# Kernel tuning notes

Measured on AMD Instinct MI355X. Metric: run time of the kernel, lower is better.

## Reference

```python
import jax, jax.numpy as jnp
import numpy as np

B, S, D, R, H = 4, 2048, 1024, 256, 8
NI, NP, NO, K = 8, 32, 8, 3
DH = R // H


def _householder_chain(x, vs):
    # x: [B,S,R], vs: [B,S,K,R]; apply K Householder reflections sequentially
    def step(carry, v):
        vn = v * jax.lax.rsqrt(jnp.sum(v * v, axis=-1, keepdims=True) + 1e-8)
        vTx = jnp.sum(carry * vn, axis=-1, keepdims=True)
        return carry - 2.0 * vn * vTx, None
    out, _ = jax.lax.scan(step, x, jnp.moveaxis(vs, 2, 0))
    return out


def _circuit_down(x, in_neurons, proc_neurons, input_weights, proc_idx):
    # soft mixture of input-neuron projections: d_model -> rank
    all_proj = jnp.einsum('bsd,ndr->bsnr', x, in_neurons)
    xr = jnp.einsum('bsnr,bsn->bsr', all_proj, input_weights)
    return _householder_chain(xr, proc_neurons[proc_idx])


def setup_inputs():
    key = jax.random.key(0)
    ks = jax.random.split(key, 14)
    n = lambda k, shape, sc: jax.random.normal(k, shape, jnp.float32) * sc
    inv_d, inv_r = 1.0 / np.sqrt(D), 1.0 / np.sqrt(R)
    return {
        'x': n(ks[0], (B, S, D), 1.0),
        'q_in': n(ks[1], (NI, D, R), inv_d),
        'q_proc': n(ks[2], (NP, R), inv_r),
        'k_in': n(ks[3], (NI, D, R), inv_d),
        'k_proc': n(ks[4], (NP, R), inv_r),
        'v_in': n(ks[5], (NI, D, R), inv_d),
        'v_proc': n(ks[6], (NP, R), inv_r),
        'o_proc': n(ks[7], (NP, R), inv_r),
        'o_out': n(ks[8], (NO, R, D), inv_r),
        'rd_in': n(ks[9], (NI, D), inv_d),
        'rd_proc': n(ks[10], (NP, D), inv_d),
        'ru_out': n(ks[11], (NO, R), inv_r),
        'ru_proc': n(ks[12], (NP, R), inv_r),
    }


def reference(x, q_in, q_proc, k_in, k_proc, v_in, v_proc, o_proc, o_out,
              rd_in, rd_proc, ru_out, ru_proc):
    # --- router (down): soft input weights + top-k process indices ---
    input_weights = jax.nn.softmax(x @ rd_in.T, axis=-1)          # [B,S,NI]
    _, pidx = jax.lax.top_k(x @ rd_proc.T, K)                     # [B,S,K]

    q = _circuit_down(x, q_in, q_proc, input_weights, pidx)      # [B,S,R]
    k = _circuit_down(x, k_in, k_proc, input_weights, pidx)
    v = _circuit_down(x, v_in, v_proc, input_weights, pidx)

    qh = q.reshape(B, S, H, DH)
    kh = k.reshape(B, S, H, DH)
    vh = v.reshape(B, S, H, DH)
    scores = jnp.einsum('bqhd,bkhd->bhqk', qh, kh) / np.sqrt(DH)
    attn = jax.nn.softmax(scores, axis=-1)
    o = jnp.einsum('bhqk,bkhd->bqhd', attn, vh).reshape(B, S, R)  # [B,S,R]

    # --- router (up): soft output weights + top-k process indices ---
    output_weights = jax.nn.softmax(o @ ru_out.T, axis=-1)        # [B,S,NO]
    _, pidx_u = jax.lax.top_k(o @ ru_proc.T, K)                   # [B,S,K]

    oh = _householder_chain(o, o_proc[pidx_u])                    # [B,S,R]
    out = jnp.einsum('bsr,bsn,nrd->bsd', oh, output_weights, o_out)
    return out
```

## Files before the change

kernel.cpp:

```cpp
#include <hip/hip_runtime.h>
#include <math.h>

#define NI 8
#define NP 32
#define TOPK 3

typedef _Float16 f16;
typedef f16 f16x8 __attribute__((ext_vector_type(8)));
typedef f16 f16x4 __attribute__((ext_vector_type(4)));
typedef float f32x4 __attribute__((ext_vector_type(4)));

__device__ __forceinline__ float wave_sum(float v) {
  #pragma unroll
  for (int off = 32; off; off >>= 1) v += __shfl_xor(v, off);
  return v;
}

__device__ __forceinline__ void gload16(const void* g, void* l) {
  __builtin_amdgcn_global_load_lds(
      (const __attribute__((address_space(1))) unsigned int*)g,
      (__attribute__((address_space(3))) unsigned int*)l, 16, 0, 0);
}

__device__ __forceinline__ void split4(float4 v, f16x4& h, f16x4& l) {
  h[0] = (f16)v.x; l[0] = (f16)(v.x - (float)h[0]);
  h[1] = (f16)v.y; l[1] = (f16)(v.y - (float)h[1]);
  h[2] = (f16)v.z; l[2] = (f16)(v.z - (float)h[2]);
  h[3] = (f16)v.w; l[3] = (f16)(v.w - (float)h[3]);
}

template<int CHUNKS>
__global__ __launch_bounds__(256) void router_v2(
    const float* __restrict__ X,
    const float* __restrict__ Wsm,
    const float* __restrict__ Wtk,
    float* __restrict__ iw, int* __restrict__ pidx,
    f16* __restrict__ Xh, f16* __restrict__ Xl)
{
  const int Kin = CHUNKS * 256;
  const int tid = threadIdx.x, wave = tid >> 6, lane = tid & 63;
  __shared__ float sc[4][4][40];
  const size_t t0 = (size_t)blockIdx.x * 16 + wave * 4;

  float4 xv[4][CHUNKS];
  #pragma unroll
  for (int tt = 0; tt < 4; ++tt) {
    const float4* Xp = reinterpret_cast<const float4*>(X + (t0 + tt) * Kin);
    #pragma unroll
    for (int c = 0; c < CHUNKS; ++c) xv[tt][c] = Xp[c * 64 + lane];
  }
  if (Xh) {
    #pragma unroll
    for (int tt = 0; tt < 4; ++tt)
      #pragma unroll
      for (int c = 0; c < CHUNKS; ++c) {
        f16x4 h, l;
        split4(xv[tt][c], h, l);
        size_t off = (t0 + tt) * Kin + (c * 64 + lane) * 4;
        *reinterpret_cast<f16x4*>(Xh + off) = h;
        *reinterpret_cast<f16x4*>(Xl + off) = l;
      }
  }

  for (int w = 0; w < 40; ++w) {
    const float* Wr = (w < NI) ? (Wsm + (size_t)w * Kin) : (Wtk + (size_t)(w - NI) * Kin);
    const float4* Wp = reinterpret_cast<const float4*>(Wr);
    float p[4] = {};
    #pragma unroll
    for (int c = 0; c < CHUNKS; ++c) {
      float4 wv = Wp[c * 64 + lane];
      #pragma unroll
      for (int tt = 0; tt < 4; ++tt) {
        p[tt] = fmaf(xv[tt][c].x, wv.x, p[tt]);
        p[tt] = fmaf(xv[tt][c].y, wv.y, p[tt]);
        p[tt] = fmaf(xv[tt][c].z, wv.z, p[tt]);
        p[tt] = fmaf(xv[tt][c].w, wv.w, p[tt]);
      }
    }
    #pragma unroll
    for (int tt = 0; tt < 4; ++tt) {
      p[tt] = wave_sum(p[tt]);
      if (lane == 0) sc[wave][tt][w] = p[tt];
    }
  }

  for (int tt = 0; tt < 4; ++tt) {
    float s = (lane < NI) ? sc[wave][tt][lane] : -3.0e38f;
    float m = s;
    #pragma unroll
    for (int off = 4; off; off >>= 1) m = fmaxf(m, __shfl_xor(m, off));
    float e = expf(s - m);
    float sum = e;
    #pragma unroll
    for (int off = 4; off; off >>= 1) sum += __shfl_xor(sum, off);
    if (lane < NI) iw[(t0 + tt) * NI + lane] = e / sum;

    float v = (lane < NP) ? sc[wave][tt][NI + lane] : -3.0e38f;
    int idx = lane;
    #pragma unroll
    for (int j = 0; j < TOPK; ++j) {
      float bv = v; int bi = idx;
      #pragma unroll
      for (int off = 32; off; off >>= 1) {
        float ov = __shfl_xor(bv, off); int oi = __shfl_xor(bi, off);
        if (ov > bv || (ov == bv && oi < bi)) { bv = ov; bi = oi; }
      }
      if (lane == 0) pidx[(t0 + tt) * TOPK + j] = bi;
      if (idx == bi) v = -3.0e38f;
    }
  }
}

__global__ __launch_bounds__(256) void pack_bt(
    const float* __restrict__ S, f16* __restrict__ Dh, f16* __restrict__ Dl,
    int C, int K)
{
  __shared__ float T[64][65];
  const int tid = threadIdx.x;
  const int kb = blockIdx.x * 64, cb = blockIdx.y * 64;
  const int tr = tid >> 4, tc = (tid & 15) * 4;
  #pragma unroll
  for (int i = 0; i < 4; ++i) {
    float4 v = *reinterpret_cast<const float4*>(&S[(size_t)(kb + tr + i * 16) * C + cb + tc]);
    T[tr + i * 16][tc + 0] = v.x; T[tr + i * 16][tc + 1] = v.y;
    T[tr + i * 16][tc + 2] = v.z; T[tr + i * 16][tc + 3] = v.w;
  }
  __syncthreads();
  #pragma unroll
  for (int i = 0; i < 4; ++i) {
    int c = tr + i * 16;
    f16x4 vh, vl;
    #pragma unroll
    for (int q = 0; q < 4; ++q) {
      float a = T[tc + q][c];
      f16 h = (f16)a;
      vh[q] = h;
      vl[q] = (f16)(a - (float)h);
    }
    *reinterpret_cast<f16x4*>(&Dh[(size_t)(cb + c) * K + kb + tc]) = vh;
    *reinterpret_cast<f16x4*>(&Dl[(size_t)(cb + c) * K + kb + tc]) = vl;
  }
}

#define TBM 128
#define TBN 128
#define TBK 32

__global__ __launch_bounds__(256, 3) void gemm_split2(
    const f16* __restrict__ Xh, const f16* __restrict__ Xl, int Kin,
    const float* __restrict__ W,
    const f16* __restrict__ Bth, const f16* __restrict__ Btl,
    float* __restrict__ C, int ldC, int Ktot, int n_pass)
{
  __shared__ f16x8 AhL[512];
  __shared__ f16x8 AlL[512];
  __shared__ f16x8 BhL[512];
  __shared__ f16x8 BlL[512];
  __shared__ float Ws[TBM][NI];

  const int tid = threadIdx.x;
  const int wave = tid >> 6, lane = tid & 63;
  const int wm = wave >> 1, wn = wave & 1;
  const int fr = lane & 15, ks = lane >> 4;
  const int row0 = blockIdx.x * TBM, c0 = blockIdx.y * TBN;
  const int n_base = blockIdx.z * n_pass;
  const int koff = n_base * Kin;

  for (int i = tid; i < TBM * NI; i += 256)
    Ws[i >> 3][i & 7] = W[(size_t)(row0 + (i >> 3)) * NI + (i & 7)];

  const int s1 = 256 + tid;
  const int ar0 = tid >> 2, kg0 = ((tid & 3) - (ar0 >> 1)) & 3;
  const int ar1 = s1 >> 2,  kg1 = ((s1 & 3) - (ar1 >> 1)) & 3;

  const f16* xh0 = Xh + (size_t)(row0 + ar0) * Kin + kg0 * 8;
  const f16* xh1 = Xh + (size_t)(row0 + ar1) * Kin + kg1 * 8;
  const f16* xl0 = Xl + (size_t)(row0 + ar0) * Kin + kg0 * 8;
  const f16* xl1 = Xl + (size_t)(row0 + ar1) * Kin + kg1 * 8;
  const f16* bh0 = Bth + (size_t)(c0 + ar0) * Ktot + koff + kg0 * 8;
  const f16* bh1 = Bth + (size_t)(c0 + ar1) * Ktot + koff + kg1 * 8;
  const f16* bl0 = Btl + (size_t)(c0 + ar0) * Ktot + koff + kg0 * 8;
  const f16* bl1 = Btl + (size_t)(c0 + ar1) * Ktot + koff + kg1 * 8;

  f16x8* AhW = &AhL[wave * 64];
  f16x8* AlW = &AlL[wave * 64];
  f16x8* BhW = &BhL[wave * 64];
  f16x8* BlW = &BlL[wave * 64];

  f32x4 acc[4][4] = {};
  f32x4 cac[4][4] = {};

  int n = n_base, dk0 = 0;
  const int Kloc = n_pass * Kin;
  for (int kt = 0; kt < Kloc; kt += TBK) {
    __syncthreads();
    gload16(xh0 + dk0, AhW);
    gload16(xh1 + dk0, AhW + 256);
    gload16(xl0 + dk0, AlW);
    gload16(xl1 + dk0, AlW + 256);
    gload16(bh0 + kt, BhW);
    gload16(bh1 + kt, BhW + 256);
    gload16(bl0 + kt, BlW);
    gload16(bl1 + kt, BlW + 256);
    __syncthreads();

    f16x8 ah[4], al[4], bh[4], bl[4];
    #pragma unroll
    for (int mf = 0; mf < 4; ++mf) {
      int ar = wm * 64 + mf * 16 + fr;
      int sl = ar * 4 + (((ar >> 1) + ks) & 3);
      ah[mf] = AhL[sl]; al[mf] = AlL[sl];
    }
    #pragma unroll
    for (int nf = 0; nf < 4; ++nf) {
      int bc = wn * 64 + nf * 16 + fr;
      int sl = bc * 4 + (((bc >> 1) + ks) & 3);
      bh[nf] = BhL[sl]; bl[nf] = BlL[sl];
    }
    #pragma unroll
    for (int mf = 0; mf < 4; ++mf)
      #pragma unroll
      for (int nf = 0; nf < 4; ++nf) {
        acc[mf][nf] = __builtin_amdgcn_mfma_f32_16x16x32_f16(ah[mf], bh[nf], acc[mf][nf], 0, 0, 0);
        acc[mf][nf] = __builtin_amdgcn_mfma_f32_16x16x32_f16(ah[mf], bl[nf], acc[mf][nf], 0, 0, 0);
        acc[mf][nf] = __builtin_amdgcn_mfma_f32_16x16x32_f16(al[mf], bh[nf], acc[mf][nf], 0, 0, 0);
      }

    dk0 += TBK;
    if (dk0 == Kin) {
      dk0 = 0;
      #pragma unroll
      for (int mf = 0; mf < 4; ++mf) {
        float w0 = Ws[wm * 64 + mf * 16 + ks * 4 + 0][n];
        float w1 = Ws[wm * 64 + mf * 16 + ks * 4 + 1][n];
        float w2 = Ws[wm * 64 + mf * 16 + ks * 4 + 2][n];
        float w3 = Ws[wm * 64 + mf * 16 + ks * 4 + 3][n];
        #pragma unroll
        for (int nf = 0; nf < 4; ++nf) {
          cac[mf][nf][0] = fmaf(w0, acc[mf][nf][0], cac[mf][nf][0]);
          cac[mf][nf][1] = fmaf(w1, acc[mf][nf][1], cac[mf][nf][1]);
          cac[mf][nf][2] = fmaf(w2, acc[mf][nf][2], cac[mf][nf][2]);
          cac[mf][nf][3] = fmaf(w3, acc[mf][nf][3], cac[mf][nf][3]);
          acc[mf][nf] = (f32x4){0.f, 0.f, 0.f, 0.f};
        }
      }
      ++n;
    }
  }

  #pragma unroll
  for (int mf = 0; mf < 4; ++mf)
    #pragma unroll
    for (int nf = 0; nf < 4; ++nf) {
      int col = c0 + wn * 64 + nf * 16 + fr;
      #pragma unroll
      for (int j = 0; j < 4; ++j) {
        int row = row0 + wm * 64 + mf * 16 + ks * 4 + j;
        atomicAdd(&C[(size_t)row * ldC + col], cac[mf][nf][j]);
      }
    }
}

#define GBM 128
#define GBN 128
#define GBK 16
#define GBMp 132

__global__ __launch_bounds__(256) void gemm_mix(
    const float* __restrict__ X, int Kin,
    const float* __restrict__ W,
    const float* __restrict__ Bm0, const float* __restrict__ Bm1, const float* __restrict__ Bm2,
    int ldB, float* __restrict__ C, int ldC, int Nz)
{
  __shared__ float As[GBK][GBMp];
  __shared__ float Bs[GBK][GBMp];
  __shared__ float Ws[GBM][NI];
  const int tid = threadIdx.x;
  const int row0 = blockIdx.x * GBM;
  const int z = blockIdx.z;
  const float* Bm = (z == 0) ? Bm0 : (z == 1) ? Bm1 : Bm2;
  const int c0 = blockIdx.y * GBN;
  for (int i = tid; i < GBM * NI; i += 256)
    Ws[i >> 3][i & 7] = W[(size_t)(row0 + (i >> 3)) * NI + (i & 7)];
  __syncthreads();

  float acc[8][8] = {};
  const int tr = tid >> 4, tc = tid & 15;
  const int srow = tid >> 2;
  const int sseg = (tid & 3) * 4;
  const int bk = tid >> 4;
  const int bc = (tid & 15) * 4;

  const int Ktot = Kin * NI;
  int n = 0, dk0 = 0;
  for (int kt = 0; kt < Ktot; kt += GBK) {
    __syncthreads();
    #pragma unroll
    for (int p = 0; p < 2; ++p) {
      int r = p * 64 + srow;
      float4 xv = *reinterpret_cast<const float4*>(&X[(size_t)(row0 + r) * Kin + dk0 + sseg]);
      float wgt = Ws[r][n];
      As[sseg + 0][r] = xv.x * wgt;
      As[sseg + 1][r] = xv.y * wgt;
      As[sseg + 2][r] = xv.z * wgt;
      As[sseg + 3][r] = xv.w * wgt;
    }
    #pragma unroll
    for (int p = 0; p < 2; ++p) {
      int cc = p * 64 + bc;
      float4 bv = *reinterpret_cast<const float4*>(&Bm[(size_t)(kt + bk) * ldB + c0 + cc]);
      *reinterpret_cast<float4*>(&Bs[bk][cc]) = bv;
    }
    __syncthreads();
    #pragma unroll
    for (int k = 0; k < GBK; ++k) {
      float4 a0 = *reinterpret_cast<const float4*>(&As[k][tr * 8]);
      float4 a1 = *reinterpret_cast<const float4*>(&As[k][tr * 8 + 4]);
      float4 b0 = *reinterpret_cast<const float4*>(&Bs[k][tc * 8]);
      float4 b1 = *reinterpret_cast<const float4*>(&Bs[k][tc * 8 + 4]);
      float av[8] = {a0.x, a0.y, a0.z, a0.w, a1.x, a1.y, a1.z, a1.w};
      float bv[8] = {b0.x, b0.y, b0.z, b0.w, b1.x, b1.y, b1.z, b1.w};
      #pragma unroll
      for (int i = 0; i < 8; ++i)
        #pragma unroll
        for (int j = 0; j < 8; ++j)
          acc[i][j] = fmaf(av[i], bv[j], acc[i][j]);
    }
    dk0 += GBK;
    if (dk0 == Kin) { dk0 = 0; ++n; }
  }
  #pragma unroll
  for (int i = 0; i < 8; ++i) {
    int row = row0 + tr * 8 + i;
    float* Cp = C + (size_t)row * ldC + z * Nz + c0 + tc * 8;
    float4 o0 = {acc[i][0], acc[i][1], acc[i][2], acc[i][3]};
    float4 o1 = {acc[i][4], acc[i][5], acc[i][6], acc[i][7]};
    *reinterpret_cast<float4*>(Cp) = o0;
    *reinterpret_cast<float4*>(Cp + 4) = o1;
  }
}

__global__ __launch_bounds__(256) void hh_kernel(
    float* __restrict__ X, int ldX,
    const float* __restrict__ P0, const float* __restrict__ P1, const float* __restrict__ P2,
    const int* __restrict__ pidx,
    f16* __restrict__ D0h, f16* __restrict__ D0l,
    f16* __restrict__ D1h, f16* __restrict__ D1l,
    f16* __restrict__ D2h, f16* __restrict__ D2l)
{
  const int tid = threadIdx.x, wave = tid >> 6, lane = tid & 63;
  const int t = blockIdx.x * 4 + wave;
  const int circ = blockIdx.y;
  const float* P = (circ == 0) ? P0 : (circ == 1) ? P1 : P2;
  float* xp = X + (size_t)t * ldX + circ * 256;
  float4 x4 = *reinterpret_cast<float4*>(xp + lane * 4);
  #pragma unroll
  for (int j = 0; j < TOPK; ++j) {
    int id = pidx[t * TOPK + j];
    const float* vp = P + (size_t)id * 256;
    float4 v4 = *reinterpret_cast<const float4*>(vp + lane * 4);
    float ss = v4.x * v4.x + v4.y * v4.y + v4.z * v4.z + v4.w * v4.w;
    ss = wave_sum(ss);
    float inv = 1.0f / sqrtf(ss + 1e-8f);
    float4 vn = {v4.x * inv, v4.y * inv, v4.z * inv, v4.w * inv};
    float dt = vn.x * x4.x + vn.y * x4.y + vn.z * x4.z + vn.w * x4.w;
    dt = wave_sum(dt);
    float d2 = 2.0f * dt;
    x4.x = fmaf(-d2, vn.x, x4.x);
    x4.y = fmaf(-d2, vn.y, x4.y);
    x4.z = fmaf(-d2, vn.z, x4.z);
    x4.w = fmaf(-d2, vn.w, x4.w);
  }
  f16* Dh = (circ == 0) ? D0h : (circ == 1) ? D1h : D2h;
  f16* Dl = (circ == 0) ? D0l : (circ == 1) ? D1l : D2l;
  if (Dh) {
    f16x4 h, l;
    split4(x4, h, l);
    *reinterpret_cast<f16x4*>(Dh + (size_t)t * 256 + lane * 4) = h;
    *reinterpret_cast<f16x4*>(Dl + (size_t)t * 256 + lane * 4) = l;
  } else {
    *reinterpret_cast<float4*>(xp + lane * 4) = x4;
  }
}

__global__ __launch_bounds__(256, 2) void attn_mfma2(
    const float* __restrict__ qkv,
    const f16* __restrict__ Khg, const f16* __restrict__ Klg,
    const f16* __restrict__ Vhg, const f16* __restrict__ Vlg,
    float* __restrict__ O)
{
  __shared__ f16 Kh[64][40], Kl[64][40];
  __shared__ f16 Vh[32][72], Vl[32][72];
  __shared__ f16 Ph[4][32][72], Pl[4][32][72];

  const int tid = threadIdx.x, wave = tid >> 6, lane = tid & 63;
  const int c = lane & 15, g = lane >> 4;
  const int bh = blockIdx.y, b = bh >> 3, h = bh & 7;
  const int q0 = blockIdx.x * 128;
  const size_t tbase = (size_t)b * 2048;
  const float SCALE = 0.17677669529663687f;

  f16x8 qh[2], ql[2];
  #pragma unroll
  for (int qt = 0; qt < 2; ++qt) {
    const int row = q0 + wave * 32 + qt * 16 + c;
    const float* qp = qkv + (tbase + row) * 768 + h * 32 + g * 8;
    float4 a = *reinterpret_cast<const float4*>(qp);
    float4 b4 = *reinterpret_cast<const float4*>(qp + 4);
    float qv[8] = {a.x, a.y, a.z, a.w, b4.x, b4.y, b4.z, b4.w};
    #pragma unroll
    for (int j = 0; j < 8; ++j) {
      float xs = qv[j] * SCALE;
      f16 hh = (f16)xs;
      qh[qt][j] = hh;
      ql[qt][j] = (f16)(xs - (float)hh);
    }
  }

  f32x4 sacc[2][4];
  f32x4 oacc[2][2] = {};
  float mrow[2][4] = {{-INFINITY, -INFINITY, -INFINITY, -INFINITY},
                      {-INFINITY, -INFINITY, -INFINITY, -INFINITY}};
  float lrow[2][4] = {};

  for (int k0 = 0; k0 < 2048; k0 += 64) {
    __syncthreads();
    {
      const int kj = tid >> 2, dq = (tid & 3) * 8;
      const size_t krow = (tbase + k0 + kj) * 256 + h * 32 + dq;
      *reinterpret_cast<f16x8*>(&Kh[kj][dq]) = *reinterpret_cast<const f16x8*>(Khg + krow);
      *reinterpret_cast<f16x8*>(&Kl[kj][dq]) = *reinterpret_cast<const f16x8*>(Klg + krow);

      const int vk = tid & 63, vq = (tid >> 6) * 8;
      const size_t vrow = (tbase + k0 + vk) * 256 + h * 32 + vq;
      f16x8 vh8 = *reinterpret_cast<const f16x8*>(Vhg + vrow);
      f16x8 vl8 = *reinterpret_cast<const f16x8*>(Vlg + vrow);
      #pragma unroll
      for (int j = 0; j < 8; ++j) { Vh[vq + j][vk] = vh8[j]; Vl[vq + j][vk] = vl8[j]; }
    }
    __syncthreads();

    #pragma unroll
    for (int s = 0; s < 4; ++s) {
      f16x8 kbh = *reinterpret_cast<const f16x8*>(&Kh[s * 16 + c][g * 8]);
      f16x8 kbl = *reinterpret_cast<const f16x8*>(&Kl[s * 16 + c][g * 8]);
      #pragma unroll
      for (int qt = 0; qt < 2; ++qt) {
        f32x4 acc = {0.f, 0.f, 0.f, 0.f};
        acc = __builtin_amdgcn_mfma_f32_16x16x32_f16(qh[qt], kbh, acc, 0, 0, 0);
        acc = __builtin_amdgcn_mfma_f32_16x16x32_f16(qh[qt], kbl, acc, 0, 0, 0);
        acc = __builtin_amdgcn_mfma_f32_16x16x32_f16(ql[qt], kbh, acc, 0, 0, 0);
        sacc[qt][s] = acc;
      }
    }

    float alpha[2][4];
    #pragma unroll
    for (int qt = 0; qt < 2; ++qt)
      #pragma unroll
      for (int r = 0; r < 4; ++r) {
        float mt = fmaxf(fmaxf(sacc[qt][0][r], sacc[qt][1][r]),
                         fmaxf(sacc[qt][2][r], sacc[qt][3][r]));
        #pragma unroll
        for (int off = 1; off < 16; off <<= 1) mt = fmaxf(mt, __shfl_xor(mt, off));
        float mn = fmaxf(mrow[qt][r], mt);
        float al = __expf(mrow[qt][r] - mn);
        mrow[qt][r] = mn;
        alpha[qt][r] = al;
        float ps = 0.f;
        #pragma unroll
        for (int s = 0; s < 4; ++s) {
          float p = __expf(sacc[qt][s][r] - mn);
          sacc[qt][s][r] = p;
          ps += p;
        }
        #pragma unroll
        for (int off = 1; off < 16; off <<= 1) ps += __shfl_xor(ps, off);
        lrow[qt][r] = lrow[qt][r] * al + ps;
      }

    #pragma unroll
    for (int qt = 0; qt < 2; ++qt)
      #pragma unroll
      for (int s = 0; s < 4; ++s)
        #pragma unroll
        for (int r = 0; r < 4; ++r) {
          float p = sacc[qt][s][r];
          f16 hh = (f16)p;
          Ph[wave][qt * 16 + g * 4 + r][s * 16 + c] = hh;
          Pl[wave][qt * 16 + g * 4 + r][s * 16 + c] = (f16)(p - (float)hh);
        }

    #pragma unroll
    for (int qt = 0; qt < 2; ++qt)
      #pragma unroll
      for (int dh = 0; dh < 2; ++dh)
        #pragma unroll
        for (int r = 0; r < 4; ++r) oacc[qt][dh][r] *= alpha[qt][r];

    #pragma unroll
    for (int ch = 0; ch < 2; ++ch) {
      f16x8 pah[2], pal[2];
      #pragma unroll
      for (int qt = 0; qt < 2; ++qt) {
        pah[qt] = *reinterpret_cast<const f16x8*>(&Ph[wave][qt * 16 + c][ch * 32 + g * 8]);
        pal[qt] = *reinterpret_cast<const f16x8*>(&Pl[wave][qt * 16 + c][ch * 32 + g * 8]);
      }
      #pragma unroll
      for (int dh = 0; dh < 2; ++dh) {
        f16x8 vh = *reinterpret_cast<const f16x8*>(&Vh[dh * 16 + c][ch * 32 + g * 8]);
        f16x8 vl = *reinterpret_cast<const f16x8*>(&Vl[dh * 16 + c][ch * 32 + g * 8]);
        #pragma unroll
        for (int qt = 0; qt < 2; ++qt) {
          oacc[qt][dh] = __builtin_amdgcn_mfma_f32_16x16x32_f16(pah[qt], vh, oacc[qt][dh], 0, 0, 0);
          oacc[qt][dh] = __builtin_amdgcn_mfma_f32_16x16x32_f16(pah[qt], vl, oacc[qt][dh], 0, 0, 0);
          oacc[qt][dh] = __builtin_amdgcn_mfma_f32_16x16x32_f16(pal[qt], vh, oacc[qt][dh], 0, 0, 0);
        }
      }
    }
  }

  #pragma unroll
  for (int qt = 0; qt < 2; ++qt)
    #pragma unroll
    for (int r = 0; r < 4; ++r) {
      float inv = 1.0f / lrow[qt][r];
      int row = q0 + wave * 32 + qt * 16 + g * 4 + r;
      #pragma unroll
      for (int dh = 0; dh < 2; ++dh)
        O[(tbase + row) * 256 + h * 32 + dh * 16 + c] = oacc[qt][dh][r] * inv;
    }
}

__global__ __launch_bounds__(256) void attn_kernel(
    const float* __restrict__ qkv, float* __restrict__ O)
{
  const int tid = threadIdx.x;
  const int wave = tid >> 6, lane = tid & 63;
  const int bh = blockIdx.y, b = bh >> 3, h = bh & 7;
  const int q0 = blockIdx.x * 8;
  const size_t tbase = (size_t)b * 2048;
  const float SCALE = 0.17677669529663687f;

  __shared__ float Ks[64][36];
  __shared__ float Vt[32][68];
  __shared__ float Ps[4][2][64];

  const int wq = __builtin_amdgcn_readfirstlane(wave);
  const float* qr0 = qkv + (tbase + q0 + wq * 2) * 768 + h * 32;
  float qa[32], qb[32];
  #pragma unroll
  for (int i = 0; i < 32; ++i) { qa[i] = qr0[i]; qb[i] = qr0[768 + i]; }

  const int r = lane >> 5, d = lane & 31;
  float m0 = -INFINITY, m1 = -INFINITY, l0 = 0.f, l1 = 0.f, oacc = 0.f;

  for (int k0 = 0; k0 < 2048; k0 += 64) {
    __syncthreads();
    {
      int j = tid >> 2;
      int c = (tid & 3) * 8;
      const float* kp = qkv + (tbase + k0 + j) * 768 + 256 + h * 32 + c;
      float4 ka = *reinterpret_cast<const float4*>(kp);
      float4 kb = *reinterpret_cast<const float4*>(kp + 4);
      *reinterpret_cast<float4*>(&Ks[j][c]) = ka;
      *reinterpret_cast<float4*>(&Ks[j][c + 4]) = kb;
      const float* vp = qkv + (tbase + k0 + j) * 768 + 512 + h * 32 + c;
      float4 va = *reinterpret_cast<const float4*>(vp);
      float4 vb = *reinterpret_cast<const float4*>(vp + 4);
      Vt[c + 0][j] = va.x; Vt[c + 1][j] = va.y; Vt[c + 2][j] = va.z; Vt[c + 3][j] = va.w;
      Vt[c + 4][j] = vb.x; Vt[c + 5][j] = vb.y; Vt[c + 6][j] = vb.z; Vt[c + 7][j] = vb.w;
    }
    __syncthreads();
    float s0 = 0.f, s1 = 0.f;
    #pragma unroll
    for (int dd = 0; dd < 8; ++dd) {
      float4 kv = *reinterpret_cast<const float4*>(&Ks[lane][dd * 4]);
      s0 = fmaf(qa[dd * 4 + 0], kv.x, s0); s1 = fmaf(qb[dd * 4 + 0], kv.x, s1);
      s0 = fmaf(qa[dd * 4 + 1], kv.y, s0); s1 = fmaf(qb[dd * 4 + 1], kv.y, s1);
      s0 = fmaf(qa[dd * 4 + 2], kv.z, s0); s1 = fmaf(qb[dd * 4 + 2], kv.z, s1);
      s0 = fmaf(qa[dd * 4 + 3], kv.w, s0); s1 = fmaf(qb[dd * 4 + 3], kv.w, s1);
    }
    s0 *= SCALE; s1 *= SCALE;
    float mx0 = s0, mx1 = s1;
    #pragma unroll
    for (int off = 32; off; off >>= 1) {
      mx0 = fmaxf(mx0, __shfl_xor(mx0, off));
      mx1 = fmaxf(mx1, __shfl_xor(mx1, off));
    }
    float nm0 = fmaxf(m0, mx0), nm1 = fmaxf(m1, mx1);
    float p0 = expf(s0 - nm0), p1 = expf(s1 - nm1);
    float a0 = expf(m0 - nm0), a1 = expf(m1 - nm1);
    float sp0 = p0, sp1 = p1;
    #pragma unroll
    for (int off = 32; off; off >>= 1) {
      sp0 += __shfl_xor(sp0, off);
      sp1 += __shfl_xor(sp1, off);
    }
    l0 = l0 * a0 + sp0; l1 = l1 * a1 + sp1;
    m0 = nm0; m1 = nm1;
    Ps[wave][0][lane] = p0; Ps[wave][1][lane] = p1;
    oacc *= (r == 0) ? a0 : a1;
    #pragma unroll
    for (int jq = 0; jq < 16; ++jq) {
      float4 pv = *reinterpret_cast<const float4*>(&Ps[wave][r][jq * 4]);
      float4 vv = *reinterpret_cast<const float4*>(&Vt[d][jq * 4]);
      oacc = fmaf(pv.x, vv.x, oacc);
      oacc = fmaf(pv.y, vv.y, oacc);
      oacc = fmaf(pv.z, vv.z, oacc);
      oacc = fmaf(pv.w, vv.w, oacc);
    }
  }
  float lf = (r == 0) ? l0 : l1;
  oacc /= lf;
  O[(tbase + q0 + wave * 2 + r) * 256 + h * 32 + d] = oacc;
}

extern "C" void kernel_launch(void* const* d_in, const int* in_sizes, int n_in,
                              void* d_out, int out_size, void* d_ws, size_t ws_size,
                              hipStream_t stream) {
  const float* x       = (const float*)d_in[0];
  const float* q_in    = (const float*)d_in[1];
  const float* q_proc  = (const float*)d_in[2];
  const float* k_in    = (const float*)d_in[3];
  const float* k_proc  = (const float*)d_in[4];
  const float* v_in    = (const float*)d_in[5];
  const float* v_proc  = (const float*)d_in[6];
  const float* o_proc  = (const float*)d_in[7];
  const float* o_out   = (const float*)d_in[8];
  const float* rd_in   = (const float*)d_in[9];
  const float* rd_proc = (const float*)d_in[10];
  const float* ru_out  = (const float*)d_in[11];
  const float* ru_proc = (const float*)d_in[12];
  float* out = (float*)d_out;
  float* qkv = (float*)d_out;

  const size_t NEED2 = (768ull << 10) + 768ull * 8192 * 2 * 2 + 8192ull * 1024 * 2 * 2;

  if (ws_size >= NEED2) {
    char* wsb = (char*)d_ws;
    float* iw    = (float*)wsb;
    float* owt   = (float*)(wsb + (256 << 10));
    int*   pidx  = (int*)(wsb + (512 << 10));
    int*   pidxu = (int*)(wsb + (640 << 10));
    char*  R1    = wsb + (768 << 10);
    f16* bth_q = (f16*)R1;
    f16* btl_q = (f16*)(R1 + 768ull * 8192 * 2);
    char*  R2    = R1 + 768ull * 8192 * 2 * 2;
    f16* Xh = (f16*)R2;
    f16* Xl = (f16*)(R2 + 8192ull * 1024 * 2);
    float* obuf  = (float*)R2;
    f16* Oh    = (f16*)(R2 + 8388608);
    f16* Ol    = (f16*)(R2 + 12582912);
    f16* bth_o = (f16*)(R2 + 16777216);
    f16* btl_o = (f16*)(R2 + 20971520);
    f16* Khg   = (f16*)(R2 + 25165824);
    f16* Klg   = (f16*)(R2 + 29360128);
    f16* Vhg = (f16*)((char*)d_out + 25165824);
    f16* Vlg = (f16*)((char*)d_out + 29360128);

    router_v2<4><<<dim3(512), dim3(256), 0, stream>>>(x, rd_in, rd_proc, iw, pidx, Xh, Xl);
    pack_bt<<<dim3(128, 4), dim3(256), 0, stream>>>(q_in, bth_q,                 btl_q,                 256, 8192);
    pack_bt<<<dim3(128, 4), dim3(256), 0, stream>>>(k_in, bth_q + 256ull * 8192, btl_q + 256ull * 8192, 256, 8192);
    pack_bt<<<dim3(128, 4), dim3(256), 0, stream>>>(v_in, bth_q + 512ull * 8192, btl_q + 512ull * 8192, 256, 8192);
    hipMemsetAsync(qkv, 0, 8192ull * 768 * 4, stream);
    gemm_split2<<<dim3(64, 6, 2), dim3(256), 0, stream>>>(Xh, Xl, 1024, iw, bth_q, btl_q,
                                                          qkv, 768, 8192, 4);
    hh_kernel<<<dim3(2048, 3), dim3(256), 0, stream>>>(qkv, 768, q_proc, k_proc, v_proc, pidx,
                                                       (f16*)nullptr, (f16*)nullptr,
                                                       Khg, Klg, Vhg, Vlg);
    pack_bt<<<dim3(32, 16), dim3(256), 0, stream>>>(o_out, bth_o, btl_o, 1024, 2048);
    attn_mfma2<<<dim3(16, 32), dim3(256), 0, stream>>>(qkv, Khg, Klg, Vhg, Vlg, obuf);
    hipMemsetAsync(d_out, 0, 8192ull * 1024 * 4, stream);
    router_v2<1><<<dim3(512), dim3(256), 0, stream>>>(obuf, ru_out, ru_proc, owt, pidxu,
                                                      (f16*)nullptr, (f16*)nullptr);
    hh_kernel<<<dim3(2048, 1), dim3(256), 0, stream>>>(obuf, 256, o_proc, o_proc, o_proc, pidxu,
                                                       Oh, Ol,
                                                       (f16*)nullptr, (f16*)nullptr,
                                                       (f16*)nullptr, (f16*)nullptr);
    gemm_split2<<<dim3(64, 8, 2), dim3(256), 0, stream>>>(Oh, Ol, 256, owt, bth_o, btl_o,
                                                          out, 1024, 2048, 4);
  } else {
    float* ws = (float*)d_ws;
    float* iw    = ws;
    int*   pidx  = (int*)(ws + 65536);
    float* obuf  = ws + 65536 + 24576;
    float* owt   = obuf + 8192 * 256;
    int*   pidxu = (int*)(owt + 65536);

    router_v2<4><<<dim3(512), dim3(256), 0, stream>>>(x, rd_in, rd_proc, iw, pidx,
                                                      (f16*)nullptr, (f16*)nullptr);
    gemm_mix<<<dim3(64, 2, 3), dim3(256), 0, stream>>>(x, 1024, iw, q_in, k_in, v_in,
                                                       256, qkv, 768, 256);
    hh_kernel<<<dim3(2048, 3), dim3(256), 0, stream>>>(qkv, 768, q_proc, k_proc, v_proc, pidx,
                                                       (f16*)nullptr, (f16*)nullptr,
                                                       (f16*)nullptr, (f16*)nullptr,
                                                       (f16*)nullptr, (f16*)nullptr);
    attn_kernel<<<dim3(256, 32), dim3(256), 0, stream>>>(qkv, obuf);
    router_v2<1><<<dim3(512), dim3(256), 0, stream>>>(obuf, ru_out, ru_proc, owt, pidxu,
                                                      (f16*)nullptr, (f16*)nullptr);
    hh_kernel<<<dim3(2048, 1), dim3(256), 0, stream>>>(obuf, 256, o_proc, o_proc, o_proc, pidxu,
                                                       (f16*)nullptr, (f16*)nullptr,
                                                       (f16*)nullptr, (f16*)nullptr,
                                                       (f16*)nullptr, (f16*)nullptr);
    gemm_mix<<<dim3(64, 8, 1), dim3(256), 0, stream>>>(obuf, 256, owt, o_out, o_out, o_out,
                                                       1024, out, 1024, 1024);
  }
}
```

Before: 830.9 us.

## Drop split-K atomics in split-f16 GEMM; use 96-wide N tiles for QKV

The split-f16 MFMA GEMM is templated on the N-fragment count and no longer splits the neuron (K) dimension across blockIdx.z. Each block now covers the full reduction and writes its output with plain stores. This removes the two memsets and the atomicAdd traffic. For the QKV projection the N tile shrinks to 96 columns so that 64x8 blocks still fill the GPU, with half the waves skipping the second B load. The cost is a longer serial K loop per block, in exchange for no atomics and no zero-fill passes.

```diff
diff --git a/kernel.cpp b/kernel.cpp
--- a/kernel.cpp
+++ b/kernel.cpp
@@ -143,19 +143,20 @@
 }
 
 #define TBM 128
-#define TBN 128
 #define TBK 32
 
+template<int NFRAG>
 __global__ __launch_bounds__(256, 3) void gemm_split2(
     const f16* __restrict__ Xh, const f16* __restrict__ Xl, int Kin,
     const float* __restrict__ W,
     const f16* __restrict__ Bth, const f16* __restrict__ Btl,
-    float* __restrict__ C, int ldC, int Ktot, int n_pass)
+    float* __restrict__ C, int ldC, int Ktot)
 {
+  const int TBN = 32 * NFRAG;
   __shared__ f16x8 AhL[512];
   __shared__ f16x8 AlL[512];
-  __shared__ f16x8 BhL[512];
-  __shared__ f16x8 BlL[512];
+  __shared__ f16x8 BhL[TBN * 4];
+  __shared__ f16x8 BlL[TBN * 4];
   __shared__ float Ws[TBM][NI];
 
   const int tid = threadIdx.x;
@@ -163,8 +164,6 @@
   const int wm = wave >> 1, wn = wave & 1;
   const int fr = lane & 15, ks = lane >> 4;
   const int row0 = blockIdx.x * TBM, c0 = blockIdx.y * TBN;
-  const int n_base = blockIdx.z * n_pass;
-  const int koff = n_base * Kin;
 
   for (int i = tid; i < TBM * NI; i += 256)
     Ws[i >> 3][i & 7] = W[(size_t)(row0 + (i >> 3)) * NI + (i & 7)];
@@ -177,34 +176,37 @@
   const f16* xh1 = Xh + (size_t)(row0 + ar1) * Kin + kg1 * 8;
   const f16* xl0 = Xl + (size_t)(row0 + ar0) * Kin + kg0 * 8;
   const f16* xl1 = Xl + (size_t)(row0 + ar1) * Kin + kg1 * 8;
-  const f16* bh0 = Bth + (size_t)(c0 + ar0) * Ktot + koff + kg0 * 8;
-  const f16* bh1 = Bth + (size_t)(c0 + ar1) * Ktot + koff + kg1 * 8;
-  const f16* bl0 = Btl + (size_t)(c0 + ar0) * Ktot + koff + kg0 * 8;
-  const f16* bl1 = Btl + (size_t)(c0 + ar1) * Ktot + koff + kg1 * 8;
+  const f16* bh0 = Bth + (size_t)(c0 + ar0) * Ktot + kg0 * 8;
+  const f16* bl0 = Btl + (size_t)(c0 + ar0) * Ktot + kg0 * 8;
+  const int ar1b = (ar1 < TBN) ? ar1 : 0;
+  const f16* bh1 = Bth + (size_t)(c0 + ar1b) * Ktot + kg1 * 8;
+  const f16* bl1 = Btl + (size_t)(c0 + ar1b) * Ktot + kg1 * 8;
+  const bool b2 = (NFRAG == 4) || (wave < 2);
 
   f16x8* AhW = &AhL[wave * 64];
   f16x8* AlW = &AlL[wave * 64];
   f16x8* BhW = &BhL[wave * 64];
   f16x8* BlW = &BlL[wave * 64];
 
-  f32x4 acc[4][4] = {};
-  f32x4 cac[4][4] = {};
-
-  int n = n_base, dk0 = 0;
-  const int Kloc = n_pass * Kin;
-  for (int kt = 0; kt < Kloc; kt += TBK) {
+  f32x4 acc[4][NFRAG] = {};
+  f32x4 cac[4][NFRAG] = {};
+
+  int n = 0, dk0 = 0;
+  for (int kt = 0; kt < Ktot; kt += TBK) {
     __syncthreads();
     gload16(xh0 + dk0, AhW);
     gload16(xh1 + dk0, AhW + 256);
     gload16(xl0 + dk0, AlW);
     gload16(xl1 + dk0, AlW + 256);
     gload16(bh0 + kt, BhW);
-    gload16(bh1 + kt, BhW + 256);
     gload16(bl0 + kt, BlW);
-    gload16(bl1 + kt, BlW + 256);
+    if (b2) {
+      gload16(bh1 + kt, BhW + 256);
+      gload16(bl1 + kt, BlW + 256);
+    }
     __syncthreads();
 
-    f16x8 ah[4], al[4], bh[4], bl[4];
+    f16x8 ah[4], al[4], bh[NFRAG], bl[NFRAG];
     #pragma unroll
     for (int mf = 0; mf < 4; ++mf) {
       int ar = wm * 64 + mf * 16 + fr;
@@ -212,15 +214,15 @@
       ah[mf] = AhL[sl]; al[mf] = AlL[sl];
     }
     #pragma unroll
-    for (int nf = 0; nf < 4; ++nf) {
-      int bc = wn * 64 + nf * 16 + fr;
+    for (int nf = 0; nf < NFRAG; ++nf) {
+      int bc = wn * (16 * NFRAG) + nf * 16 + fr;
       int sl = bc * 4 + (((bc >> 1) + ks) & 3);
       bh[nf] = BhL[sl]; bl[nf] = BlL[sl];
     }
     #pragma unroll
     for (int mf = 0; mf < 4; ++mf)
       #pragma unroll
-      for (int nf = 0; nf < 4; ++nf) {
+      for (int nf = 0; nf < NFRAG; ++nf) {
         acc[mf][nf] = __builtin_amdgcn_mfma_f32_16x16x32_f16(ah[mf], bh[nf], acc[mf][nf], 0, 0, 0);
         acc[mf][nf] = __builtin_amdgcn_mfma_f32_16x16x32_f16(ah[mf], bl[nf], acc[mf][nf], 0, 0, 0);
         acc[mf][nf] = __builtin_amdgcn_mfma_f32_16x16x32_f16(al[mf], bh[nf], acc[mf][nf], 0, 0, 0);
@@ -236,7 +238,7 @@
         float w2 = Ws[wm * 64 + mf * 16 + ks * 4 + 2][n];
         float w3 = Ws[wm * 64 + mf * 16 + ks * 4 + 3][n];
         #pragma unroll
-        for (int nf = 0; nf < 4; ++nf) {
+        for (int nf = 0; nf < NFRAG; ++nf) {
           cac[mf][nf][0] = fmaf(w0, acc[mf][nf][0], cac[mf][nf][0]);
           cac[mf][nf][1] = fmaf(w1, acc[mf][nf][1], cac[mf][nf][1]);
           cac[mf][nf][2] = fmaf(w2, acc[mf][nf][2], cac[mf][nf][2]);
@@ -251,12 +253,12 @@
   #pragma unroll
   for (int mf = 0; mf < 4; ++mf)
     #pragma unroll
-    for (int nf = 0; nf < 4; ++nf) {
-      int col = c0 + wn * 64 + nf * 16 + fr;
+    for (int nf = 0; nf < NFRAG; ++nf) {
+      int col = c0 + wn * (16 * NFRAG) + nf * 16 + fr;
       #pragma unroll
       for (int j = 0; j < 4; ++j) {
         int row = row0 + wm * 64 + mf * 16 + ks * 4 + j;
-        atomicAdd(&C[(size_t)row * ldC + col], cac[mf][nf][j]);
+        C[(size_t)row * ldC + col] = cac[mf][nf][j];
       }
     }
 }
@@ -663,23 +665,21 @@
     pack_bt<<<dim3(128, 4), dim3(256), 0, stream>>>(q_in, bth_q,                 btl_q,                 256, 8192);
     pack_bt<<<dim3(128, 4), dim3(256), 0, stream>>>(k_in, bth_q + 256ull * 8192, btl_q + 256ull * 8192, 256, 8192);
     pack_bt<<<dim3(128, 4), dim3(256), 0, stream>>>(v_in, bth_q + 512ull * 8192, btl_q + 512ull * 8192, 256, 8192);
-    hipMemsetAsync(qkv, 0, 8192ull * 768 * 4, stream);
-    gemm_split2<<<dim3(64, 6, 2), dim3(256), 0, stream>>>(Xh, Xl, 1024, iw, bth_q, btl_q,
-                                                          qkv, 768, 8192, 4);
+    gemm_split2<3><<<dim3(64, 8), dim3(256), 0, stream>>>(Xh, Xl, 1024, iw, bth_q, btl_q,
+                                                          qkv, 768, 8192);
     hh_kernel<<<dim3(2048, 3), dim3(256), 0, stream>>>(qkv, 768, q_proc, k_proc, v_proc, pidx,
                                                        (f16*)nullptr, (f16*)nullptr,
                                                        Khg, Klg, Vhg, Vlg);
     pack_bt<<<dim3(32, 16), dim3(256), 0, stream>>>(o_out, bth_o, btl_o, 1024, 2048);
     attn_mfma2<<<dim3(16, 32), dim3(256), 0, stream>>>(qkv, Khg, Klg, Vhg, Vlg, obuf);
-    hipMemsetAsync(d_out, 0, 8192ull * 1024 * 4, stream);
     router_v2<1><<<dim3(512), dim3(256), 0, stream>>>(obuf, ru_out, ru_proc, owt, pidxu,
                                                       (f16*)nullptr, (f16*)nullptr);
     hh_kernel<<<dim3(2048, 1), dim3(256), 0, stream>>>(obuf, 256, o_proc, o_proc, o_proc, pidxu,
                                                        Oh, Ol,
                                                        (f16*)nullptr, (f16*)nullptr,
                                                        (f16*)nullptr, (f16*)nullptr);
-    gemm_split2<<<dim3(64, 8, 2), dim3(256), 0, stream>>>(Oh, Ol, 256, owt, bth_o, btl_o,
-                                                          out, 1024, 2048, 4);
+    gemm_split2<4><<<dim3(64, 8), dim3(256), 0, stream>>>(Oh, Ol, 256, owt, bth_o, btl_o,
+                                                          out, 1024, 2048);
   } else {
     float* ws = (float*)d_ws;
     float* iw    = ws;
```

After: 743.5 us. 1.12x faster.
